# Kernel optimization log

Measured on AMD Instinct MI355X. Metric: run time of the kernel, lower is better.

The kernel has to match this reference:

```python
import jax, jax.numpy as jnp
import numpy as np

B, C, H, W, MODES, RANK = 16, 128, 128, 128, 16, 8


def setup_inputs() -> dict:
    key = jax.random.key(0)
    ks = jax.random.split(key, 8)
    scale = 1.0 / (C * C)
    lr_scale = 0.02
    return {
        "x": jax.random.normal(ks[0], (B, C, H, W), dtype=jnp.float32),
        "w_real": scale * jax.random.normal(ks[1], (C, C, MODES, MODES), dtype=jnp.float32),
        "w_imag": scale * jax.random.normal(ks[2], (C, C, MODES, MODES), dtype=jnp.float32),
        "u_real": lr_scale * jax.random.normal(ks[3], (C, RANK, MODES, MODES), dtype=jnp.float32),
        "u_imag": lr_scale * jax.random.normal(ks[4], (C, RANK, MODES, MODES), dtype=jnp.float32),
        "v_real": lr_scale * jax.random.normal(ks[5], (C, RANK, MODES, MODES), dtype=jnp.float32),
        "v_imag": lr_scale * jax.random.normal(ks[6], (C, RANK, MODES, MODES), dtype=jnp.float32),
        "skip_w": (1.0 / np.sqrt(C)) * jax.random.normal(ks[7], (C, C), dtype=jnp.float32),
    }


def physical_act(x):
    # f(x) = x * exp(-|x|^2)
    return x * jnp.exp(-jnp.abs(x) ** 2)


def reference(x, w_real, w_imag, u_real, u_imag, v_real, v_imag, skip_w):
    Bb, Cc, Hh, Ww = x.shape
    # 1x1 conv skip path == channel matmul
    x_skip = jnp.einsum('oc,bchw->bohw', skip_w, x)
    # FFT to spectral domain: (B, C, H, W//2+1) complex64
    x_ft = jnp.fft.rfft2(x, norm='ortho')
    W_ft = x_ft.shape[-1]
    m1 = min(w_real.shape[-2], Hh)
    m2 = min(w_real.shape[-1], W_ft)
    # truncated-mode complex diagonal operator D (per-frequency channel mix)
    D = (w_real + 1j * w_imag)[:, :, :m1, :m2]          # (O, I, m1, m2)
    x_top = x_ft[:, :, :m1, :m2]                         # (B, I, m1, m2)
    out_top = jnp.einsum('bimn,oimn->bomn', x_top, D)
    # low-rank cross-frequency mixer UV*
    U = (u_real + 1j * u_imag)[:, :, :m1, :m2]           # (O, R, m1, m2)
    V = (v_real + 1j * v_imag)[:, :, :m1, :m2]           # (I, R, m1, m2)
    z = jnp.einsum('bimn,irmn->br', x_top, jnp.conj(V))  # (B, R)
    out_top = out_top + jnp.einsum('ormn,br->bomn', U, z)
    # scatter back into zero-padded full spectrum
    out_ft = jnp.zeros(x_ft.shape, dtype=x_ft.dtype).at[:, :, :m1, :m2].set(out_top)
    x_spectral = jnp.fft.irfft2(out_ft, s=(Hh, Ww), norm='ortho')
    out = x_spectral + x_skip
    return physical_act(out)
```

## Files before the change

### kernel.cpp

```cpp
#include <hip/hip_runtime.h>
#include <math.h>

#define TAB_OFF 0
#define XTOP_OFF 16384
#define Z_OFF (16384 + 1048576)
#define OTOP_OFF (Z_OFF + 256)
#define TF_OFF (OTOP_OFF + 1048576)
#define SWF_OFF XTOP_OFF


using bf16x8 = __attribute__((ext_vector_type(8))) short;
using s16x4  = __attribute__((ext_vector_type(4))) short;
using f32x16 = __attribute__((ext_vector_type(16))) float;

__device__ inline unsigned short bf_rnd(float v) {
  return (unsigned short)((__float_as_uint(v) + 0x8000u) >> 16);
}
__device__ inline void bf_split(float v, unsigned short& hi, unsigned short& lo) {
  unsigned u = __float_as_uint(v);
  hi = (unsigned short)(u >> 16);
  float r = v - __uint_as_float(u & 0xFFFF0000u);
  lo = (unsigned short)(__float_as_uint(r) >> 16);
}
__device__ inline bf16x8 ldfrag(const unsigned short* p) {
  s16x4 a = *(const s16x4*)p;
  s16x4 b = *(const s16x4*)(p + 4);
  bf16x8 r;
  r[0] = a[0]; r[1] = a[1]; r[2] = a[2]; r[3] = a[3];
  r[4] = b[0]; r[5] = b[1]; r[6] = b[2]; r[7] = b[3];
  return r;
}
__device__ inline bf16x8 ldfrag_sw(const unsigned short* base, int row, int koff) {
  int byte = row * 256 + ((koff * 2) ^ ((row & 7) << 4));
  return ldfrag((const unsigned short*)((const char*)base + byte));
}

__global__ __launch_bounds__(256) void k_tab(float* __restrict__ tab) {
  int idx = blockIdx.x * 256 + threadIdx.x;
  if (idx >= 16384) return;
  int which = idx >> 11, rem = idx & 2047;
  int a, j;
  if (which == 4 || which == 5) { a = rem & 127; j = rem >> 7; }
  else { a = rem >> 4; j = rem & 15; }
  int p = (a * j) & 127;
  float ang = (float)p * (float)(3.14159265358979323846 / 64.0);
  float cv = cosf(ang), sv = sinf(ang);
  float v;
  switch (which) {
    case 0: v = cv * (1.f / 128.f); break;
    case 1: v = -sv * (1.f / 128.f); break;
    case 2: v = cv; break;
    case 3: v = sv; break;
    case 4: v = cv; break;
    case 5: v = sv; break;
    case 6: v = ((rem & 15) == 0 ? 1.f : 2.f) * cv * (1.f / 128.f); break;
    default: v = ((rem & 15) == 0 ? 1.f : 2.f) * (-sv) * (1.f / 128.f); break;
  }
  tab[idx] = v;
}

__global__ __launch_bounds__(256) void k_fprep(unsigned short* __restrict__ tf) {
  int idx = blockIdx.x * 256 + threadIdx.x;
  if (idx >= 4096) return;
  int np = idx >> 7, k = idx & 127;
  int n = np & 15;
  int p = (k * n) & 127;
  float ang = (float)p * (float)(3.14159265358979323846 / 64.0);
  float v = (np < 16 ? cosf(ang) : -sinf(ang)) * (1.f / 128.f);
  unsigned short hi, lo;
  bf_split(v, hi, lo);
  tf[np * 128 + k] = hi;
  tf[4096 + np * 128 + k] = lo;
}

__global__ __launch_bounds__(256) void k_wprep(const float* __restrict__ sw,
                                               unsigned short* __restrict__ swf) {
  int idx = blockIdx.x * 256 + threadIdx.x;
  if (idx >= 16384) return;
  int o = idx >> 7, k = idx & 127;
  unsigned short hb, lb;
  bf_split(sw[o * 128 + k], hb, lb);
  int kc = k >> 5, ks = (k >> 4) & 1, kh = (k >> 3) & 1, j = k & 7;
  int f0 = (kc * 2 + ks) * 2;
  swf[(f0 + 0) * 2048 + o * 16 + kh * 8 + j] = hb;
  swf[(f0 + 1) * 2048 + o * 16 + kh * 8 + j] = lb;
}

__global__ __launch_bounds__(256) void k_fwd(const float* __restrict__ x,
                                             const unsigned short* __restrict__ tf,
                                             const float* __restrict__ tab,
                                             float* __restrict__ xtop) {
  __shared__ unsigned short Xh[128 * 128];
  __shared__ unsigned short Tfh[32 * 128];
  __shared__ unsigned short Tfl[32 * 128];
  const int c = blockIdx.x, b = blockIdx.y;
  const int t = threadIdx.x;
  const int lane = t & 63, wv = t >> 6;

  #pragma unroll
  for (int it = 0; it < 32; ++it) {
    int idx = it * 256 + t;
    int part = idx >> 12, rem = idx & 4095;
    int row = rem >> 7, k = rem & 127;
    unsigned short v = tf[part * 4096 + rem];
    unsigned short* dst = part ? Tfl : Tfh;
    *(unsigned short*)((char*)dst + row * 256 + ((k * 2) ^ ((row & 7) << 4))) = v;
  }
  const float* img = x + (((size_t)(b * 128 + c)) << 14);
  #pragma unroll
  for (int it = 0; it < 16; ++it) {
    int flat = it * 256 + t;
    int h = flat >> 5, wq = flat & 31;
    float4 v = *(const float4*)(img + (size_t)flat * 4);
    s16x4 pk;
    pk[0] = (short)bf_rnd(v.x); pk[1] = (short)bf_rnd(v.y);
    pk[2] = (short)bf_rnd(v.z); pk[3] = (short)bf_rnd(v.w);
    *(s16x4*)((char*)Xh + h * 256 + ((wq * 8) ^ ((h & 7) << 4))) = pk;
  }
  __syncthreads();

  f32x16 acc;
  #pragma unroll
  for (int e = 0; e < 16; ++e) acc[e] = 0.f;
  const int orow = wv * 32 + (lane & 31);
  const int bcol = lane & 31;
  const int kh8 = (lane >> 5) * 8;
  #pragma unroll
  for (int kc8 = 0; kc8 < 8; ++kc8) {
    int kfull = kc8 * 16 + kh8;
    bf16x8 a  = ldfrag_sw(Xh, orow, kfull);
    bf16x8 th = ldfrag_sw(Tfh, bcol, kfull);
    bf16x8 tl = ldfrag_sw(Tfl, bcol, kfull);
    acc = __builtin_amdgcn_mfma_f32_32x32x16_bf16(a, th, acc, 0, 0, 0);
    acc = __builtin_amdgcn_mfma_f32_32x32x16_bf16(a, tl, acc, 0, 0, 0);
  }
  __syncthreads();

  float* Arp = (float*)Xh;
  float* Aip = Arp + 16 * 132;
  {
    const int col = lane & 31;
    #pragma unroll
    for (int r = 0; r < 16; ++r) {
      int h = wv * 32 + (r & 3) + 8 * (r >> 2) + 4 * (lane >> 5);
      if (col < 16) Arp[col * 132 + h] = acc[r];
      else          Aip[(col - 16) * 132 + h] = acc[r];
    }
  }
  __syncthreads();

  {
    const int m = t >> 4, n = t & 15;
    const float* tc = tab + 8192 + m * 128;
    const float* ts = tab + 10240 + m * 128;
    const float* ar = Arp + n * 132;
    const float* ai = Aip + n * 132;
    float xr = 0.f, xi = 0.f;
    #pragma unroll 8
    for (int h4 = 0; h4 < 128; h4 += 4) {
      float4 av = *(const float4*)(ar + h4);
      float4 iv = *(const float4*)(ai + h4);
      float4 cv = *(const float4*)(tc + h4);
      float4 sv = *(const float4*)(ts + h4);
      xr += av.x * cv.x + iv.x * sv.x;  xi += iv.x * cv.x - av.x * sv.x;
      xr += av.y * cv.y + iv.y * sv.y;  xi += iv.y * cv.y - av.y * sv.y;
      xr += av.z * cv.z + iv.z * sv.z;  xi += iv.z * cv.z - av.z * sv.z;
      xr += av.w * cv.w + iv.w * sv.w;  xi += iv.w * cv.w - av.w * sv.w;
    }
    size_t base = ((size_t)(b * 128 + c)) * 512 + (size_t)(m * 16 + n) * 2;
    xtop[base] = xr; xtop[base + 1] = xi;
  }
}

__global__ __launch_bounds__(256) void k_z(const float* __restrict__ xtop,
                                           const float* __restrict__ vre,
                                           const float* __restrict__ vim,
                                           float* __restrict__ zout) {
  int b = blockIdx.x, ic = blockIdx.y, t = threadIdx.x;
  float zr[8], zi[8];
  #pragma unroll
  for (int r = 0; r < 8; ++r) { zr[r] = 0.f; zi[r] = 0.f; }
  const float* xb = xtop + ((size_t)b * 128) * 512;
  for (int i = ic * 16; i < ic * 16 + 16; ++i) {
    float xr = xb[i * 512 + t * 2], xi = xb[i * 512 + t * 2 + 1];
    #pragma unroll
    for (int r = 0; r < 8; ++r) {
      float vr = vre[(size_t)(i * 8 + r) * 256 + t];
      float vi = vim[(size_t)(i * 8 + r) * 256 + t];
      zr[r] += xr * vr + xi * vi;
      zi[r] += xi * vr - xr * vi;
    }
  }
  #pragma unroll
  for (int r = 0; r < 8; ++r)
    for (int off = 32; off > 0; off >>= 1) {
      zr[r] += __shfl_down(zr[r], off);
      zi[r] += __shfl_down(zi[r], off);
    }
  __shared__ float red[4][16];
  int wid = t >> 6, lane = t & 63;
  if (lane == 0) {
    #pragma unroll
    for (int r = 0; r < 8; ++r) { red[wid][r * 2] = zr[r]; red[wid][r * 2 + 1] = zi[r]; }
  }
  __syncthreads();
  if (t < 16) atomicAdd(&zout[b * 16 + t], red[0][t] + red[1][t] + red[2][t] + red[3][t]);
}

__global__ __launch_bounds__(256) void k_mix(const float* __restrict__ xtop,
                                             const float* __restrict__ wre,
                                             const float* __restrict__ wim,
                                             const float* __restrict__ ure,
                                             const float* __restrict__ uim,
                                             const float* __restrict__ z,
                                             float* __restrict__ otop) {
  int o0 = blockIdx.x * 4, b0 = blockIdx.y * 2, ic = blockIdx.z, t = threadIdx.x;
  float ar[2][4], ai[2][4];
  #pragma unroll
  for (int bb = 0; bb < 2; ++bb)
    #pragma unroll
    for (int oo = 0; oo < 4; ++oo) { ar[bb][oo] = 0.f; ai[bb][oo] = 0.f; }
  const float* x0 = xtop + ((size_t)(b0 * 128)) * 512;
  const float* x1 = x0 + 128 * 512;
  for (int i = ic * 16; i < ic * 16 + 16; ++i) {
    float x0r = x0[i * 512 + t * 2], x0i = x0[i * 512 + t * 2 + 1];
    float x1r = x1[i * 512 + t * 2], x1i = x1[i * 512 + t * 2 + 1];
    #pragma unroll
    for (int oo = 0; oo < 4; ++oo) {
      size_t di = (size_t)((o0 + oo) * 128 + i) * 256 + t;
      float dr = wre[di], dj = wim[di];
      ar[0][oo] += dr * x0r - dj * x0i; ai[0][oo] += dr * x0i + dj * x0r;
      ar[1][oo] += dr * x1r - dj * x1i; ai[1][oo] += dr * x1i + dj * x1r;
    }
  }
  if (ic == 0) {
    float zr[2][8], zi[2][8];
    #pragma unroll
    for (int bb = 0; bb < 2; ++bb)
      #pragma unroll
      for (int r = 0; r < 8; ++r) {
        zr[bb][r] = z[(b0 + bb) * 16 + r * 2];
        zi[bb][r] = z[(b0 + bb) * 16 + r * 2 + 1];
      }
    #pragma unroll
    for (int oo = 0; oo < 4; ++oo)
      #pragma unroll
      for (int r = 0; r < 8; ++r) {
        float urv = ure[(size_t)((o0 + oo) * 8 + r) * 256 + t];
        float uiv = uim[(size_t)((o0 + oo) * 8 + r) * 256 + t];
        #pragma unroll
        for (int bb = 0; bb < 2; ++bb) {
          ar[bb][oo] += urv * zr[bb][r] - uiv * zi[bb][r];
          ai[bb][oo] += urv * zi[bb][r] + uiv * zr[bb][r];
        }
      }
  }
  #pragma unroll
  for (int bb = 0; bb < 2; ++bb)
    #pragma unroll
    for (int oo = 0; oo < 4; ++oo) {
      size_t oi = ((size_t)((b0 + bb) * 128 + o0 + oo) * 256 + (size_t)t) * 2;
      atomicAdd(&otop[oi], ar[bb][oo]);
      atomicAdd(&otop[oi + 1], ai[bb][oo]);
    }
}

__global__ __launch_bounds__(256) void k_out(const float* __restrict__ x,
                                             const unsigned short* __restrict__ swf,
                                             const float* __restrict__ otop,
                                             const float* __restrict__ tab,
                                             float* __restrict__ out) {
  __shared__ unsigned short Ylds[128 * 36];
  __shared__ unsigned short Tlds[128 * 36];
  __shared__ unsigned short Bh[128 * 36], Bl[128 * 36];
  const int h = blockIdx.x, b = blockIdx.y;
  const int t = threadIdx.x;
  const int lane = t & 63, wv = t >> 6;
  const int kh8 = (lane >> 5) * 8;
  const int o_lane = wv * 32 + (lane & 31);

  {
    int w = t >> 1, half = t & 1;
    const float* src = tab + (half ? 14336 : 12288) + w * 16;
    #pragma unroll
    for (int q = 0; q < 4; ++q) {
      float4 v = *(const float4*)(src + q * 4);
      int k0 = half * 16 + q * 4;
      Tlds[w * 36 + k0 + 0] = bf_rnd(v.x);
      Tlds[w * 36 + k0 + 1] = bf_rnd(v.y);
      Tlds[w * 36 + k0 + 2] = bf_rnd(v.z);
      Tlds[w * 36 + k0 + 3] = bf_rnd(v.w);
    }
  }
  {
    int o = t >> 1, nh = (t & 1) * 8;
    float yr[8], yi[8];
    #pragma unroll
    for (int j = 0; j < 8; ++j) { yr[j] = 0.f; yi[j] = 0.f; }
    const float* xb = otop + ((size_t)(b * 128 + o)) * 512 + nh * 2;
    #pragma unroll 4
    for (int m = 0; m < 16; ++m) {
      float cm = tab[4096 + h * 16 + m];
      float sm = tab[6144 + h * 16 + m];
      float4 q0 = *(const float4*)(xb + m * 32 + 0);
      float4 q1 = *(const float4*)(xb + m * 32 + 4);
      float4 q2 = *(const float4*)(xb + m * 32 + 8);
      float4 q3 = *(const float4*)(xb + m * 32 + 12);
      yr[0] += q0.x * cm - q0.y * sm; yi[0] += q0.x * sm + q0.y * cm;
      yr[1] += q0.z * cm - q0.w * sm; yi[1] += q0.z * sm + q0.w * cm;
      yr[2] += q1.x * cm - q1.y * sm; yi[2] += q1.x * sm + q1.y * cm;
      yr[3] += q1.z * cm - q1.w * sm; yi[3] += q1.z * sm + q1.w * cm;
      yr[4] += q2.x * cm - q2.y * sm; yi[4] += q2.x * sm + q2.y * cm;
      yr[5] += q2.z * cm - q2.w * sm; yi[5] += q2.z * sm + q2.w * cm;
      yr[6] += q3.x * cm - q3.y * sm; yi[6] += q3.x * sm + q3.y * cm;
      yr[7] += q3.z * cm - q3.w * sm; yi[7] += q3.z * sm + q3.w * cm;
    }
    #pragma unroll
    for (int j = 0; j < 8; ++j) {
      Ylds[o * 36 + nh + j] = bf_rnd(yr[j]);
      Ylds[o * 36 + 16 + nh + j] = bf_rnd(yi[j]);
    }
  }
  __syncthreads();

  f32x16 acc[4];
  #pragma unroll
  for (int nt = 0; nt < 4; ++nt)
    #pragma unroll
    for (int e = 0; e < 16; ++e) acc[nt][e] = 0.f;

  for (int kc = 0; kc < 4; ++kc) {
    float xv[16];
    #pragma unroll
    for (int it = 0; it < 16; ++it) {
      int c = kc * 32 + it * 2 + (t >> 7);
      int w = t & 127;
      xv[it] = x[(size_t)(b * 128 + c) * 16384 + (size_t)h * 128 + w];
    }
    bf16x8 ah[2], al[2];
    #pragma unroll
    for (int ks = 0; ks < 2; ++ks) {
      const unsigned short* base = swf + (size_t)((kc * 2 + ks) * 2) * 2048 + o_lane * 16 + kh8;
      ah[ks] = *(const bf16x8*)base;
      al[ks] = *(const bf16x8*)(base + 2048);
    }
    __syncthreads();
    #pragma unroll
    for (int it = 0; it < 16; ++it) {
      int cl = it * 2 + (t >> 7);
      int w = t & 127;
      unsigned short hb, lb;
      bf_split(xv[it], hb, lb);
      Bh[w * 36 + cl] = hb; Bl[w * 36 + cl] = lb;
    }
    __syncthreads();
    #pragma unroll
    for (int ks = 0; ks < 2; ++ks) {
      const int kb = ks * 16 + kh8;
      #pragma unroll
      for (int nt = 0; nt < 4; ++nt) {
        bf16x8 bh_ = ldfrag(&Bh[(nt * 32 + (lane & 31)) * 36 + kb]);
        bf16x8 bl_ = ldfrag(&Bl[(nt * 32 + (lane & 31)) * 36 + kb]);
        acc[nt] = __builtin_amdgcn_mfma_f32_32x32x16_bf16(ah[ks], bh_, acc[nt], 0, 0, 0);
        acc[nt] = __builtin_amdgcn_mfma_f32_32x32x16_bf16(ah[ks], bl_, acc[nt], 0, 0, 0);
        acc[nt] = __builtin_amdgcn_mfma_f32_32x32x16_bf16(al[ks], bh_, acc[nt], 0, 0, 0);
      }
    }
  }

  #pragma unroll
  for (int ks = 0; ks < 2; ++ks) {
    const int kb = ks * 16 + kh8;
    bf16x8 ya = ldfrag(&Ylds[o_lane * 36 + kb]);
    #pragma unroll
    for (int nt = 0; nt < 4; ++nt) {
      bf16x8 tb = ldfrag(&Tlds[(nt * 32 + (lane & 31)) * 36 + kb]);
      acc[nt] = __builtin_amdgcn_mfma_f32_32x32x16_bf16(ya, tb, acc[nt], 0, 0, 0);
    }
  }

  #pragma unroll
  for (int nt = 0; nt < 4; ++nt) {
    int w = nt * 32 + (lane & 31);
    #pragma unroll
    for (int r = 0; r < 16; ++r) {
      int o = wv * 32 + (r & 3) + 8 * (r >> 2) + 4 * (lane >> 5);
      float v = acc[nt][r];
      out[((size_t)(b * 128 + o)) * 16384 + (size_t)h * 128 + w] = v * __expf(-v * v);
    }
  }
}

extern "C" void kernel_launch(void* const* d_in, const int* in_sizes, int n_in,
                              void* d_out, int out_size, void* d_ws, size_t ws_size,
                              hipStream_t stream) {
  const float* x  = (const float*)d_in[0];
  const float* wr = (const float*)d_in[1];
  const float* wi = (const float*)d_in[2];
  const float* ur = (const float*)d_in[3];
  const float* ui = (const float*)d_in[4];
  const float* vr = (const float*)d_in[5];
  const float* vi = (const float*)d_in[6];
  const float* sw = (const float*)d_in[7];
  float* out  = (float*)d_out;
  float* ws   = (float*)d_ws;
  float* tab  = ws + TAB_OFF;
  float* xtop = ws + XTOP_OFF;
  float* z    = ws + Z_OFF;
  float* otop = ws + OTOP_OFF;
  unsigned short* tf  = (unsigned short*)(ws + TF_OFF);
  unsigned short* swf = (unsigned short*)(ws + SWF_OFF);

  hipMemsetAsync(z, 0, 256 * sizeof(float), stream);
  hipMemsetAsync(otop, 0, 1048576 * sizeof(float), stream);
  hipLaunchKernelGGL(k_tab, dim3(64), dim3(256), 0, stream, tab);
  hipLaunchKernelGGL(k_fprep, dim3(16), dim3(256), 0, stream, tf);
  hipLaunchKernelGGL(k_fwd, dim3(128, 16), dim3(256), 0, stream, x, tf, tab, xtop);
  hipLaunchKernelGGL(k_z,   dim3(16, 8), dim3(256), 0, stream, xtop, vr, vi, z);
  hipLaunchKernelGGL(k_mix, dim3(32, 8, 8), dim3(256), 0, stream, xtop, wr, wi, ur, ui, z, otop);
  hipLaunchKernelGGL(k_wprep, dim3(64), dim3(256), 0, stream, sw, swf);
  hipLaunchKernelGGL(k_out, dim3(128, 16), dim3(256), 0, stream, x, swf, otop, tab, out);
}
```

Baseline: 202.2 us.

## Load skip-path x fragments directly into MFMA registers, dropping LDS staging in k_out

Reworks k_out so each wave owns 32 columns of w and all 128 output channels. Each lane reads x straight from global memory into its MFMA B fragment and splits it into bf16 hi/lo in registers, which removes the Bh/Bl LDS staging and the per-chunk barriers. The inverse-DFT twiddle table is now precomputed once in bf16 fragment layout by a new k_t2prep kernel and read from global memory instead of being built in LDS per block. The cost is strided global loads across channels and more swf weight-fragment loads per wave, since each wave now reads all four output tiles.

```diff
diff --git a/kernel.cpp b/kernel.cpp
--- a/kernel.cpp
+++ b/kernel.cpp
@@ -6,6 +6,7 @@
 #define Z_OFF (16384 + 1048576)
 #define OTOP_OFF (Z_OFF + 256)
 #define TF_OFF (OTOP_OFF + 1048576)
+#define T2F_OFF (TF_OFF + 4096)
 #define SWF_OFF XTOP_OFF
 
 
@@ -73,6 +74,15 @@
   tf[4096 + np * 128 + k] = lo;
 }
 
+__global__ __launch_bounds__(256) void k_t2prep(const float* __restrict__ tab,
+                                                unsigned short* __restrict__ t2f) {
+  int idx = blockIdx.x * 256 + threadIdx.x;
+  if (idx >= 4096) return;
+  int w = idx >> 5, np = idx & 31;
+  float v = (np < 16) ? tab[12288 + w * 16 + np] : tab[14336 + w * 16 + (np - 16)];
+  t2f[idx] = bf_rnd(v);
+}
+
 __global__ __launch_bounds__(256) void k_wprep(const float* __restrict__ sw,
                                                unsigned short* __restrict__ swf) {
   int idx = blockIdx.x * 256 + threadIdx.x;
@@ -267,31 +277,18 @@
 
 __global__ __launch_bounds__(256) void k_out(const float* __restrict__ x,
                                              const unsigned short* __restrict__ swf,
+                                             const unsigned short* __restrict__ t2f,
                                              const float* __restrict__ otop,
                                              const float* __restrict__ tab,
                                              float* __restrict__ out) {
   __shared__ unsigned short Ylds[128 * 36];
-  __shared__ unsigned short Tlds[128 * 36];
-  __shared__ unsigned short Bh[128 * 36], Bl[128 * 36];
   const int h = blockIdx.x, b = blockIdx.y;
   const int t = threadIdx.x;
   const int lane = t & 63, wv = t >> 6;
   const int kh8 = (lane >> 5) * 8;
-  const int o_lane = wv * 32 + (lane & 31);
-
-  {
-    int w = t >> 1, half = t & 1;
-    const float* src = tab + (half ? 14336 : 12288) + w * 16;
-    #pragma unroll
-    for (int q = 0; q < 4; ++q) {
-      float4 v = *(const float4*)(src + q * 4);
-      int k0 = half * 16 + q * 4;
-      Tlds[w * 36 + k0 + 0] = bf_rnd(v.x);
-      Tlds[w * 36 + k0 + 1] = bf_rnd(v.y);
-      Tlds[w * 36 + k0 + 2] = bf_rnd(v.z);
-      Tlds[w * 36 + k0 + 3] = bf_rnd(v.w);
-    }
-  }
+  const int col = lane & 31;
+  const int w0 = wv * 32;
+
   {
     int o = t >> 1, nh = (t & 1) * 8;
     float yr[8], yi[8];
@@ -325,68 +322,54 @@
 
   f32x16 acc[4];
   #pragma unroll
-  for (int nt = 0; nt < 4; ++nt)
-    #pragma unroll
-    for (int e = 0; e < 16; ++e) acc[nt][e] = 0.f;
-
-  for (int kc = 0; kc < 4; ++kc) {
-    float xv[16];
-    #pragma unroll
-    for (int it = 0; it < 16; ++it) {
-      int c = kc * 32 + it * 2 + (t >> 7);
-      int w = t & 127;
-      xv[it] = x[(size_t)(b * 128 + c) * 16384 + (size_t)h * 128 + w];
-    }
-    bf16x8 ah[2], al[2];
-    #pragma unroll
-    for (int ks = 0; ks < 2; ++ks) {
-      const unsigned short* base = swf + (size_t)((kc * 2 + ks) * 2) * 2048 + o_lane * 16 + kh8;
-      ah[ks] = *(const bf16x8*)base;
-      al[ks] = *(const bf16x8*)(base + 2048);
-    }
-    __syncthreads();
-    #pragma unroll
-    for (int it = 0; it < 16; ++it) {
-      int cl = it * 2 + (t >> 7);
-      int w = t & 127;
+  for (int ot = 0; ot < 4; ++ot)
+    #pragma unroll
+    for (int e = 0; e < 16; ++e) acc[ot][e] = 0.f;
+
+  const float* xb = x + (size_t)b * 2097152 + (size_t)h * 128 + (w0 + col);
+  #pragma unroll
+  for (int ks8 = 0; ks8 < 8; ++ks8) {
+    const int c0 = ks8 * 16 + kh8;
+    float xd[8];
+    #pragma unroll
+    for (int j = 0; j < 8; ++j) xd[j] = xb[(size_t)(c0 + j) * 16384];
+    bf16x8 bh, bl;
+    #pragma unroll
+    for (int j = 0; j < 8; ++j) {
       unsigned short hb, lb;
-      bf_split(xv[it], hb, lb);
-      Bh[w * 36 + cl] = hb; Bl[w * 36 + cl] = lb;
-    }
-    __syncthreads();
-    #pragma unroll
-    for (int ks = 0; ks < 2; ++ks) {
-      const int kb = ks * 16 + kh8;
-      #pragma unroll
-      for (int nt = 0; nt < 4; ++nt) {
-        bf16x8 bh_ = ldfrag(&Bh[(nt * 32 + (lane & 31)) * 36 + kb]);
-        bf16x8 bl_ = ldfrag(&Bl[(nt * 32 + (lane & 31)) * 36 + kb]);
-        acc[nt] = __builtin_amdgcn_mfma_f32_32x32x16_bf16(ah[ks], bh_, acc[nt], 0, 0, 0);
-        acc[nt] = __builtin_amdgcn_mfma_f32_32x32x16_bf16(ah[ks], bl_, acc[nt], 0, 0, 0);
-        acc[nt] = __builtin_amdgcn_mfma_f32_32x32x16_bf16(al[ks], bh_, acc[nt], 0, 0, 0);
-      }
+      bf_split(xd[j], hb, lb);
+      bh[j] = (short)hb; bl[j] = (short)lb;
+    }
+    const unsigned short* abase = swf + ks8 * 4096 + kh8;
+    #pragma unroll
+    for (int ot = 0; ot < 4; ++ot) {
+      const int o = ot * 32 + col;
+      bf16x8 ah = *(const bf16x8*)(abase + o * 16);
+      bf16x8 al = *(const bf16x8*)(abase + 2048 + o * 16);
+      acc[ot] = __builtin_amdgcn_mfma_f32_32x32x16_bf16(ah, bh, acc[ot], 0, 0, 0);
+      acc[ot] = __builtin_amdgcn_mfma_f32_32x32x16_bf16(ah, bl, acc[ot], 0, 0, 0);
+      acc[ot] = __builtin_amdgcn_mfma_f32_32x32x16_bf16(al, bh, acc[ot], 0, 0, 0);
     }
   }
 
   #pragma unroll
   for (int ks = 0; ks < 2; ++ks) {
     const int kb = ks * 16 + kh8;
-    bf16x8 ya = ldfrag(&Ylds[o_lane * 36 + kb]);
-    #pragma unroll
-    for (int nt = 0; nt < 4; ++nt) {
-      bf16x8 tb = ldfrag(&Tlds[(nt * 32 + (lane & 31)) * 36 + kb]);
-      acc[nt] = __builtin_amdgcn_mfma_f32_32x32x16_bf16(ya, tb, acc[nt], 0, 0, 0);
-    }
-  }
-
-  #pragma unroll
-  for (int nt = 0; nt < 4; ++nt) {
-    int w = nt * 32 + (lane & 31);
+    bf16x8 tb = *(const bf16x8*)(t2f + (w0 + col) * 32 + kb);
+    #pragma unroll
+    for (int ot = 0; ot < 4; ++ot) {
+      bf16x8 ya = ldfrag(&Ylds[(ot * 32 + col) * 36 + kb]);
+      acc[ot] = __builtin_amdgcn_mfma_f32_32x32x16_bf16(ya, tb, acc[ot], 0, 0, 0);
+    }
+  }
+
+  #pragma unroll
+  for (int ot = 0; ot < 4; ++ot) {
     #pragma unroll
     for (int r = 0; r < 16; ++r) {
-      int o = wv * 32 + (r & 3) + 8 * (r >> 2) + 4 * (lane >> 5);
-      float v = acc[nt][r];
-      out[((size_t)(b * 128 + o)) * 16384 + (size_t)h * 128 + w] = v * __expf(-v * v);
+      int o = ot * 32 + (r & 3) + 8 * (r >> 2) + 4 * (lane >> 5);
+      float v = acc[ot][r];
+      out[((size_t)(b * 128 + o)) * 16384 + (size_t)h * 128 + w0 + col] = v * __expf(-v * v);
     }
   }
 }
@@ -409,15 +392,17 @@
   float* z    = ws + Z_OFF;
   float* otop = ws + OTOP_OFF;
   unsigned short* tf  = (unsigned short*)(ws + TF_OFF);
+  unsigned short* t2f = (unsigned short*)(ws + T2F_OFF);
   unsigned short* swf = (unsigned short*)(ws + SWF_OFF);
 
   hipMemsetAsync(z, 0, 256 * sizeof(float), stream);
   hipMemsetAsync(otop, 0, 1048576 * sizeof(float), stream);
   hipLaunchKernelGGL(k_tab, dim3(64), dim3(256), 0, stream, tab);
   hipLaunchKernelGGL(k_fprep, dim3(16), dim3(256), 0, stream, tf);
+  hipLaunchKernelGGL(k_t2prep, dim3(16), dim3(256), 0, stream, tab, t2f);
   hipLaunchKernelGGL(k_fwd, dim3(128, 16), dim3(256), 0, stream, x, tf, tab, xtop);
   hipLaunchKernelGGL(k_z,   dim3(16, 8), dim3(256), 0, stream, xtop, vr, vi, z);
   hipLaunchKernelGGL(k_mix, dim3(32, 8, 8), dim3(256), 0, stream, xtop, wr, wi, ur, ui, z, otop);
   hipLaunchKernelGGL(k_wprep, dim3(64), dim3(256), 0, stream, sw, swf);
-  hipLaunchKernelGGL(k_out, dim3(128, 16), dim3(256), 0, stream, x, swf, otop, tab, out);
-}
+  hipLaunchKernelGGL(k_out, dim3(128, 16), dim3(256), 0, stream, x, swf, t2f, otop, tab, out);
+}
```

Measured after the change: 207.6 us. 2.7% more time.

## Prefetch next x chunk in k_out and precompute bf16 inverse-DFT table

Applied to the files above, without the earlier changes.

The k_out channel loop now register-prefetches the next 32-channel slice of x while MFMAs run on the current slice. It drops one of the two barriers per iteration by moving the bf16 split-and-store before the weight loads and adding a trailing barrier. The per-block conversion of the inverse DFT twiddle table into LDS is replaced by a tiny prep kernel that writes a bf16 table once, which k_out reads straight from global memory. This shrinks LDS use and per-block prologue work, but adds an extra launch and more register pressure from the xn buffer.

```diff
diff --git a/kernel.cpp b/kernel.cpp
--- a/kernel.cpp
+++ b/kernel.cpp
@@ -6,8 +6,8 @@
 #define Z_OFF (16384 + 1048576)
 #define OTOP_OFF (Z_OFF + 256)
 #define TF_OFF (OTOP_OFF + 1048576)
+#define T2F_OFF (TF_OFF + 4096)
 #define SWF_OFF XTOP_OFF
-
 
 using bf16x8 = __attribute__((ext_vector_type(8))) short;
 using s16x4  = __attribute__((ext_vector_type(4))) short;
@@ -73,6 +73,15 @@
   tf[4096 + np * 128 + k] = lo;
 }
 
+__global__ __launch_bounds__(256) void k_t2prep(const float* __restrict__ tab,
+                                                unsigned short* __restrict__ t2f) {
+  int idx = blockIdx.x * 256 + threadIdx.x;
+  if (idx >= 4096) return;
+  int w = idx >> 5, np = idx & 31;
+  float v = (np < 16) ? tab[12288 + w * 16 + np] : tab[14336 + w * 16 + (np - 16)];
+  t2f[idx] = bf_rnd(v);
+}
+
 __global__ __launch_bounds__(256) void k_wprep(const float* __restrict__ sw,
                                                unsigned short* __restrict__ swf) {
   int idx = blockIdx.x * 256 + threadIdx.x;
@@ -267,31 +276,27 @@
 
 __global__ __launch_bounds__(256) void k_out(const float* __restrict__ x,
                                              const unsigned short* __restrict__ swf,
+                                             const unsigned short* __restrict__ t2f,
                                              const float* __restrict__ otop,
                                              const float* __restrict__ tab,
                                              float* __restrict__ out) {
   __shared__ unsigned short Ylds[128 * 36];
-  __shared__ unsigned short Tlds[128 * 36];
   __shared__ unsigned short Bh[128 * 36], Bl[128 * 36];
   const int h = blockIdx.x, b = blockIdx.y;
   const int t = threadIdx.x;
   const int lane = t & 63, wv = t >> 6;
   const int kh8 = (lane >> 5) * 8;
-  const int o_lane = wv * 32 + (lane & 31);
-
-  {
-    int w = t >> 1, half = t & 1;
-    const float* src = tab + (half ? 14336 : 12288) + w * 16;
-    #pragma unroll
-    for (int q = 0; q < 4; ++q) {
-      float4 v = *(const float4*)(src + q * 4);
-      int k0 = half * 16 + q * 4;
-      Tlds[w * 36 + k0 + 0] = bf_rnd(v.x);
-      Tlds[w * 36 + k0 + 1] = bf_rnd(v.y);
-      Tlds[w * 36 + k0 + 2] = bf_rnd(v.z);
-      Tlds[w * 36 + k0 + 3] = bf_rnd(v.w);
-    }
-  }
+  const int col = lane & 31;
+  const int o_lane = wv * 32 + col;
+
+  const int cofs = t >> 7;
+  const int wB = t & 127;
+  const float* xbase = x + (size_t)b * 2097152 + (size_t)h * 128 + wB;
+  float xv[16], xn[16];
+  #pragma unroll
+  for (int it = 0; it < 16; ++it)
+    xv[it] = xbase[(size_t)(it * 2 + cofs) * 16384];
+
   {
     int o = t >> 1, nh = (t & 1) * 8;
     float yr[8], yi[8];
@@ -329,13 +334,16 @@
     #pragma unroll
     for (int e = 0; e < 16; ++e) acc[nt][e] = 0.f;
 
+  #pragma unroll
   for (int kc = 0; kc < 4; ++kc) {
-    float xv[16];
-    #pragma unroll
-    for (int it = 0; it < 16; ++it) {
-      int c = kc * 32 + it * 2 + (t >> 7);
-      int w = t & 127;
-      xv[it] = x[(size_t)(b * 128 + c) * 16384 + (size_t)h * 128 + w];
+    {
+      #pragma unroll
+      for (int it = 0; it < 16; ++it) {
+        int cl = it * 2 + cofs;
+        unsigned short hb, lb;
+        bf_split(xv[it], hb, lb);
+        Bh[wB * 36 + cl] = hb; Bl[wB * 36 + cl] = lb;
+      }
     }
     bf16x8 ah[2], al[2];
     #pragma unroll
@@ -344,14 +352,10 @@
       ah[ks] = *(const bf16x8*)base;
       al[ks] = *(const bf16x8*)(base + 2048);
     }
-    __syncthreads();
-    #pragma unroll
-    for (int it = 0; it < 16; ++it) {
-      int cl = it * 2 + (t >> 7);
-      int w = t & 127;
-      unsigned short hb, lb;
-      bf_split(xv[it], hb, lb);
-      Bh[w * 36 + cl] = hb; Bl[w * 36 + cl] = lb;
+    if (kc < 3) {
+      #pragma unroll
+      for (int it = 0; it < 16; ++it)
+        xn[it] = xbase[(size_t)((kc + 1) * 32 + it * 2 + cofs) * 16384];
     }
     __syncthreads();
     #pragma unroll
@@ -359,13 +363,18 @@
       const int kb = ks * 16 + kh8;
       #pragma unroll
       for (int nt = 0; nt < 4; ++nt) {
-        bf16x8 bh_ = ldfrag(&Bh[(nt * 32 + (lane & 31)) * 36 + kb]);
-        bf16x8 bl_ = ldfrag(&Bl[(nt * 32 + (lane & 31)) * 36 + kb]);
+        bf16x8 bh_ = ldfrag(&Bh[(nt * 32 + col) * 36 + kb]);
+        bf16x8 bl_ = ldfrag(&Bl[(nt * 32 + col) * 36 + kb]);
         acc[nt] = __builtin_amdgcn_mfma_f32_32x32x16_bf16(ah[ks], bh_, acc[nt], 0, 0, 0);
         acc[nt] = __builtin_amdgcn_mfma_f32_32x32x16_bf16(ah[ks], bl_, acc[nt], 0, 0, 0);
         acc[nt] = __builtin_amdgcn_mfma_f32_32x32x16_bf16(al[ks], bh_, acc[nt], 0, 0, 0);
       }
     }
+    __syncthreads();
+    if (kc < 3) {
+      #pragma unroll
+      for (int it = 0; it < 16; ++it) xv[it] = xn[it];
+    }
   }
 
   #pragma unroll
@@ -374,14 +383,14 @@
     bf16x8 ya = ldfrag(&Ylds[o_lane * 36 + kb]);
     #pragma unroll
     for (int nt = 0; nt < 4; ++nt) {
-      bf16x8 tb = ldfrag(&Tlds[(nt * 32 + (lane & 31)) * 36 + kb]);
+      bf16x8 tb = *(const bf16x8*)(t2f + (nt * 32 + col) * 32 + kb);
       acc[nt] = __builtin_amdgcn_mfma_f32_32x32x16_bf16(ya, tb, acc[nt], 0, 0, 0);
     }
   }
 
   #pragma unroll
   for (int nt = 0; nt < 4; ++nt) {
-    int w = nt * 32 + (lane & 31);
+    int w = nt * 32 + col;
     #pragma unroll
     for (int r = 0; r < 16; ++r) {
       int o = wv * 32 + (r & 3) + 8 * (r >> 2) + 4 * (lane >> 5);
@@ -409,15 +418,17 @@
   float* z    = ws + Z_OFF;
   float* otop = ws + OTOP_OFF;
   unsigned short* tf  = (unsigned short*)(ws + TF_OFF);
+  unsigned short* t2f = (unsigned short*)(ws + T2F_OFF);
   unsigned short* swf = (unsigned short*)(ws + SWF_OFF);
 
   hipMemsetAsync(z, 0, 256 * sizeof(float), stream);
   hipMemsetAsync(otop, 0, 1048576 * sizeof(float), stream);
   hipLaunchKernelGGL(k_tab, dim3(64), dim3(256), 0, stream, tab);
   hipLaunchKernelGGL(k_fprep, dim3(16), dim3(256), 0, stream, tf);
+  hipLaunchKernelGGL(k_t2prep, dim3(16), dim3(256), 0, stream, tab, t2f);
   hipLaunchKernelGGL(k_fwd, dim3(128, 16), dim3(256), 0, stream, x, tf, tab, xtop);
   hipLaunchKernelGGL(k_z,   dim3(16, 8), dim3(256), 0, stream, xtop, vr, vi, z);
   hipLaunchKernelGGL(k_mix, dim3(32, 8, 8), dim3(256), 0, stream, xtop, wr, wi, ur, ui, z, otop);
   hipLaunchKernelGGL(k_wprep, dim3(64), dim3(256), 0, stream, sw, swf);
-  hipLaunchKernelGGL(k_out, dim3(128, 16), dim3(256), 0, stream, x, swf, otop, tab, out);
-}
+  hipLaunchKernelGGL(k_out, dim3(128, 16), dim3(256), 0, stream, x, swf, t2f, otop, tab, out);
+}
```

Result: no change. 204.3 us (+1.0%).
